# Kernel tuning notes

Hardware: AMD Instinct MI355X
Metric: run time of the kernel (lower is better)

Reference implementation:

```python
import jax, jax.numpy as jnp
import numpy as np

V = 512          # num vertices
F = 64           # pair-feature dim (gpnn_channels in)
C = 64           # gpnn_channels out
E = 8192         # num edges (avg degree 16)


def setup_inputs() -> dict:
    key = jax.random.key(0)
    k1, k2, k3, k4 = jax.random.split(key, 4)
    alpha = jax.random.normal(k1, (V * V, F), dtype=jnp.float32)          # pair features, row v*V+w
    edge_index = jax.random.randint(k2, (2, E), 0, V)                      # COO [src; dst]
    # GPNNEdgeConv.nn = MLP([F, C, C], act='relu')  (norm treated as identity / eval stats)
    w1 = jax.random.normal(k3, (F, C), dtype=jnp.float32) * (1.0 / np.sqrt(F))
    b1 = jnp.zeros((C,), dtype=jnp.float32)
    w2 = jax.random.normal(k4, (C, C), dtype=jnp.float32) * (1.0 / np.sqrt(C))
    b2 = jnp.zeros((C,), dtype=jnp.float32)
    eps = jnp.asarray(0.0, dtype=jnp.float32)                              # train_eps parameter
    return {"alpha": alpha, "edge_index": edge_index,
            "w1": w1, "b1": b1, "w2": w2, "b2": b2, "eps": eps}


def reference(alpha, edge_index, w1, b1, w2, b2, eps):
    # Dense 0/1 adjacency adj_t: adj[v, j] = 1 iff edge j -> v (dst-indexed, as spmm(adj_t, .)).
    adj = jnp.zeros((V, V), dtype=alpha.dtype).at[edge_index[1], edge_index[0]].set(1.0)
    a3 = alpha.reshape(V, V, F)  # a3[v, j] = alpha[v*V + j]
    # message_and_aggregate: out[v*V+w] = row v of spmm(adj_t, A_{v,w}),
    # where A_{v,w}[j] = alpha[v*V+j] + alpha[w*V+j]  (sum aggregation)
    #   = sum_j adj[v,j] * (a3[v,j] + a3[w,j]) = S[v] + T[v,w]
    S = jnp.einsum('vj,vjf->vf', adj, a3)    # [V, F]
    T = jnp.einsum('vj,wjf->vwf', adj, a3)   # [V, V, F]
    out = (S[:, None, :] + T).reshape(V * V, F)
    # GINConv residual: out + (1 + eps) * x_r, then MLP (Linear-ReLU-Linear)
    out = out + (1.0 + eps) * alpha
    h = jax.nn.relu(out @ w1 + b1)
    return h @ w2 + b2
```

## Files before the change

kernel.cpp:

```cpp
#include <hip/hip_runtime.h>
#include <hip/hip_bf16.h>

#define NV 512
#define NF 64

typedef __attribute__((ext_vector_type(8))) short bf16x8;
typedef __attribute__((ext_vector_type(4))) float f32x4;

union BF8 { bf16x8 v; unsigned u[4]; };

__device__ __forceinline__ unsigned short f2bf(float x) {
    unsigned u = __float_as_uint(x);
    unsigned r = (u + 0x7fffu + ((u >> 16) & 1u)) >> 16;
    return (unsigned short)r;
}

__device__ __forceinline__ unsigned awt_addr(int f, int jbyte) {
    return (unsigned)((f * 1024 + jbyte) ^ (((f ^ (f >> 3)) & 7) << 4));
}
__device__ __forceinline__ unsigned wt_addr(int m, int n, int kbyte) {
    return (unsigned)(m * 8192 + ((n * 128 + kbyte) ^ (((n ^ (n >> 3)) & 7) << 4)));
}

__global__ void k_edges(const int* __restrict__ ei, int E, unsigned int* __restrict__ mask) {
    int e = blockIdx.x * 256 + threadIdx.x;
    if (e < E) {
        int s = ei[e];
        int d = ei[E + e];
        atomicOr(&mask[d * 16 + (s >> 5)], 1u << (s & 31));
    }
}

__global__ void k_S(const unsigned int* __restrict__ mask, const float* __restrict__ alpha,
                    float* __restrict__ S) {
    __shared__ float red[4][64];
    int v = blockIdx.x;
    int lane = threadIdx.x & 63;
    int g = threadIdx.x >> 6;
    float a0 = 0.f, a1 = 0.f;
    for (int wd = g * 4; wd < g * 4 + 4; ++wd) {
        unsigned bits = mask[v * 16 + wd];
        while (bits) {
            int b0 = __ffs(bits) - 1; bits &= bits - 1;
            float x0 = alpha[((size_t)v * NV + wd * 32 + b0) * NF + lane];
            if (bits) {
                int b1 = __ffs(bits) - 1; bits &= bits - 1;
                a1 += alpha[((size_t)v * NV + wd * 32 + b1) * NF + lane];
            }
            a0 += x0;
        }
    }
    red[g][lane] = a0 + a1;
    __syncthreads();
    if (g == 0)
        S[v * NF + lane] = red[0][lane] + red[1][lane] + red[2][lane] + red[3][lane];
}

#define SCR_OFF 65536

__global__ __launch_bounds__(512, 4) void k_main(
    const float* __restrict__ alpha, const float* __restrict__ w1, const float* __restrict__ b1,
    const float* __restrict__ w2, const float* __restrict__ b2, const float* __restrict__ eps_p,
    const unsigned int* __restrict__ mask, const float* __restrict__ S,
    float* __restrict__ out)
{
    extern __shared__ char smem[];

    const int w    = blockIdx.x;
    const int t    = threadIdx.x;
    const int lane = t & 63;
    const int wid  = t >> 6;
    const int nlo  = lane & 15;
    const int g    = lane >> 4;
    const int mbase = wid * 64;
    const float* src = alpha + (size_t)w * (NV * NF);

    auto stage_half = [&](int i) {
        int task = i * 512 + t;
        int jb = task >> 4;
        int fq = task & 15;
        unsigned ua[4][4];
#pragma unroll
        for (int h = 0; h < 4; ++h) {
            f32x4 r0 = *(const f32x4*)(src + (size_t)(jb * 8 + 2 * h) * NF + fq * 4);
            f32x4 r1 = *(const f32x4*)(src + (size_t)(jb * 8 + 2 * h + 1) * NF + fq * 4);
#pragma unroll
            for (int c = 0; c < 4; ++c)
                ua[c][h] = (unsigned)f2bf(r0[c]) | ((unsigned)f2bf(r1[c]) << 16);
        }
#pragma unroll
        for (int c = 0; c < 4; ++c) {
            BF8 p;
            p.u[0] = ua[c][0]; p.u[1] = ua[c][1]; p.u[2] = ua[c][2]; p.u[3] = ua[c][3];
            *(bf16x8*)(smem + awt_addr(fq * 4 + c, jb * 16)) = p.v;
        }
    };

    f32x4 acc[4][4];

    stage_half(0);

#pragma unroll
    for (int mi = 0; mi < 4; ++mi)
#pragma unroll
        for (int nt = 0; nt < 4; ++nt)
#pragma unroll
            for (int r = 0; r < 4; ++r)
                acc[mi][nt][r] = S[(size_t)(mbase + mi * 16 + g * 4 + r) * NF + nt * 16 + nlo];

    __syncthreads();

    auto gemm_q = [&](int kq) {
        unsigned qw[4][4];
#pragma unroll
        for (int mi = 0; mi < 4; ++mi) {
            const uint4 q = *(const uint4*)(mask + (size_t)(mbase + mi * 16 + nlo) * 16 + kq * 4);
            qw[mi][0] = q.x; qw[mi][1] = q.y; qw[mi][2] = q.z; qw[mi][3] = q.w;
        }
#pragma unroll
        for (int kr = 0; kr < 4; ++kr) {
            const int kk = kq * 4 + kr;
            BF8 afr[4];
#pragma unroll
            for (int mi = 0; mi < 4; ++mi) {
                unsigned byteb = (qw[mi][kr] >> (g * 8)) & 0xFFu;
#pragma unroll
                for (int h = 0; h < 4; ++h) {
                    unsigned b0 = (byteb >> (2 * h)) & 1u;
                    unsigned b1 = (byteb >> (2 * h + 1)) & 1u;
                    afr[mi].u[h] = (b0 ? 0x3F80u : 0u) | (b1 ? 0x3F800000u : 0u);
                }
            }
#pragma unroll
            for (int nt = 0; nt < 4; ++nt) {
                bf16x8 bfr = *(const bf16x8*)(smem + awt_addr(nt * 16 + nlo, kk * 64 + g * 16));
#pragma unroll
                for (int mi = 0; mi < 4; ++mi)
                    acc[mi][nt] = __builtin_amdgcn_mfma_f32_16x16x32_bf16(afr[mi].v, bfr, acc[mi][nt], 0, 0, 0);
            }
        }
    };

    stage_half(1);
    gemm_q(0);
    gemm_q(1);
    __syncthreads();
    gemm_q(2);
    gemm_q(3);
    __syncthreads();

    if (t < 256) {
        int m  = t >> 7;
        int sub = t & 127;
        int jb = sub >> 4;
        int fq = sub & 15;
        const float* wsrc = m ? w2 : w1;
        unsigned ua[4][4];
#pragma unroll
        for (int h = 0; h < 4; ++h) {
            f32x4 r0 = *(const f32x4*)(wsrc + (size_t)(jb * 8 + 2 * h) * NF + fq * 4);
            f32x4 r1 = *(const f32x4*)(wsrc + (size_t)(jb * 8 + 2 * h + 1) * NF + fq * 4);
#pragma unroll
            for (int c = 0; c < 4; ++c)
                ua[c][h] = (unsigned)f2bf(r0[c]) | ((unsigned)f2bf(r1[c]) << 16);
        }
#pragma unroll
        for (int c = 0; c < 4; ++c) {
            BF8 p;
            p.u[0] = ua[c][0]; p.u[1] = ua[c][1]; p.u[2] = ua[c][2]; p.u[3] = ua[c][3];
            *(bf16x8*)(smem + wt_addr(m, fq * 4 + c, jb * 16)) = p.v;
        }
    }
    float b1v[4], b2v[4];
#pragma unroll
    for (int nt = 0; nt < 4; ++nt) {
        b1v[nt] = b1[nt * 16 + nlo];
        b2v[nt] = b2[nt * 16 + nlo];
    }
    const float ceps = 1.0f + eps_p[0];

    __syncthreads();

    char* myscr = smem + SCR_OFF + wid * 2048;
#pragma unroll
    for (int mi = 0; mi < 4; ++mi) {
        int v0 = mbase + mi * 16;

        float rvv[4][4];
#pragma unroll
        for (int nt = 0; nt < 4; ++nt)
#pragma unroll
            for (int r = 0; r < 4; ++r)
                rvv[nt][r] = alpha[((size_t)(v0 + g * 4 + r) * NV + w) * NF + nt * 16 + nlo];

#pragma unroll
        for (int nt = 0; nt < 4; ++nt) {
            int f = nt * 16 + nlo;
#pragma unroll
            for (int r = 0; r < 4; ++r) {
                float pre = acc[mi][nt][r] + ceps * rvv[nt][r];
                int row = g * 4 + r;
                *(unsigned short*)(myscr + row * 128 + ((2 * f) ^ ((row & 7) << 4))) = f2bf(pre);
            }
        }

        bf16x8 a0 = *(const bf16x8*)(myscr + nlo * 128 + ((g * 16) ^ ((nlo & 7) << 4)));
        bf16x8 a1 = *(const bf16x8*)(myscr + nlo * 128 + ((g * 16 + 64) ^ ((nlo & 7) << 4)));
        f32x4 accm[4];
#pragma unroll
        for (int nt = 0; nt < 4; ++nt) {
            bf16x8 wf0 = *(const bf16x8*)(smem + wt_addr(0, nt * 16 + nlo, g * 16));
            bf16x8 wf1 = *(const bf16x8*)(smem + wt_addr(0, nt * 16 + nlo, 64 + g * 16));
            f32x4 z = {0.f, 0.f, 0.f, 0.f};
            z = __builtin_amdgcn_mfma_f32_16x16x32_bf16(a0, wf0, z, 0, 0, 0);
            z = __builtin_amdgcn_mfma_f32_16x16x32_bf16(a1, wf1, z, 0, 0, 0);
            accm[nt] = z;
        }

#pragma unroll
        for (int nt = 0; nt < 4; ++nt)
#pragma unroll
            for (int r = 0; r < 4; ++r) {
                float hv = accm[nt][r] + b1v[nt];
                hv = hv > 0.f ? hv : 0.f;
                int row = g * 4 + r;
                *(unsigned short*)(myscr + row * 128 + ((2 * (nt * 16 + nlo)) ^ ((row & 7) << 4))) = f2bf(hv);
            }

        bf16x8 h0 = *(const bf16x8*)(myscr + nlo * 128 + ((g * 16) ^ ((nlo & 7) << 4)));
        bf16x8 h1 = *(const bf16x8*)(myscr + nlo * 128 + ((g * 16 + 64) ^ ((nlo & 7) << 4)));
#pragma unroll
        for (int nt = 0; nt < 4; ++nt) {
            bf16x8 wf0 = *(const bf16x8*)(smem + wt_addr(1, nt * 16 + nlo, g * 16));
            bf16x8 wf1 = *(const bf16x8*)(smem + wt_addr(1, nt * 16 + nlo, 64 + g * 16));
            f32x4 z = {0.f, 0.f, 0.f, 0.f};
            z = __builtin_amdgcn_mfma_f32_16x16x32_bf16(h0, wf0, z, 0, 0, 0);
            z = __builtin_amdgcn_mfma_f32_16x16x32_bf16(h1, wf1, z, 0, 0, 0);
#pragma unroll
            for (int r = 0; r < 4; ++r) {
                int vv = v0 + g * 4 + r;
                __builtin_nontemporal_store(z[r] + b2v[nt],
                    out + ((size_t)vv * NV + w) * NF + nt * 16 + nlo);
            }
        }
    }
}

extern "C" void kernel_launch(void* const* d_in, const int* in_sizes, int n_in,
                              void* d_out, int out_size, void* d_ws, size_t ws_size,
                              hipStream_t stream) {
    const float* alpha = (const float*)d_in[0];
    const int*   ei    = (const int*)d_in[1];
    const float* w1    = (const float*)d_in[2];
    const float* b1    = (const float*)d_in[3];
    const float* w2    = (const float*)d_in[4];
    const float* b2    = (const float*)d_in[5];
    const float* eps   = (const float*)d_in[6];
    float* out = (float*)d_out;
    int E = in_sizes[1] / 2;

    unsigned int* mask = (unsigned int*)d_ws;
    float* S = (float*)d_ws + 8192;

    hipMemsetAsync(mask, 0, 8192 * sizeof(unsigned int), stream);
    k_edges<<<(E + 255) / 256, 256, 0, stream>>>(ei, E, mask);
    k_S    <<<NV, 256, 0, stream>>>(mask, alpha, S);

    const int smem_bytes = 81920;
    hipFuncSetAttribute(reinterpret_cast<const void*>(k_main),
                        hipFuncAttributeMaxDynamicSharedMemorySize, smem_bytes);
    k_main <<<NV, 512, smem_bytes, stream>>>(alpha, w1, b1, w2, b2, eps, mask, S, out);
}
```

Before: 73.20 us.

## Prefetch residual rows, reswizzle scratch, shrink LDS, use plain output stores

The epilogue now loads the residual alpha rows for the next 16-row tile before processing the current one, so global loads overlap the MFMA work. The scratch area moves to offset 16384, reusing LDS that appears free after the main loop, which cuts dynamic shared memory from 80KB to 64KB and may allow more resident blocks. The scratch swizzle changes to a new slot function meant to reduce bank conflicts on the 2-byte transposing writes. Nontemporal output stores become ordinary stores. The risks are higher register pressure from the double-buffered residual and possible aliasing if the reused LDS region is still live.

```diff
diff --git a/kernel.cpp b/kernel.cpp
--- a/kernel.cpp
+++ b/kernel.cpp
@@ -20,6 +20,9 @@
 }
 __device__ __forceinline__ unsigned wt_addr(int m, int n, int kbyte) {
     return (unsigned)(m * 8192 + ((n * 128 + kbyte) ^ (((n ^ (n >> 3)) & 7) << 4)));
+}
+__device__ __forceinline__ int scr_slot(int row) {
+    return ((row >> 2) ^ ((row & 3) << 1)) & 7;
 }
 
 __global__ void k_edges(const int* __restrict__ ei, int E, unsigned int* __restrict__ mask) {
@@ -56,7 +59,6 @@
         S[v * NF + lane] = red[0][lane] + red[1][lane] + red[2][lane] + red[3][lane];
 }
 
-#define SCR_OFF 65536
 
 __global__ __launch_bounds__(512, 4) void k_main(
     const float* __restrict__ alpha, const float* __restrict__ w1, const float* __restrict__ b1,
@@ -179,33 +181,47 @@
     }
     const float ceps = 1.0f + eps_p[0];
 
-    __syncthreads();
-
-    char* myscr = smem + SCR_OFF + wid * 2048;
+    float rvv[4][4];
+#pragma unroll
+    for (int nt = 0; nt < 4; ++nt)
+#pragma unroll
+        for (int r = 0; r < 4; ++r)
+            rvv[nt][r] = alpha[((size_t)(mbase + g * 4 + r) * NV + w) * NF + nt * 16 + nlo];
+
+    __syncthreads();
+
+    char* myscr = smem + 16384 + wid * 2048;
 #pragma unroll
     for (int mi = 0; mi < 4; ++mi) {
         int v0 = mbase + mi * 16;
 
-        float rvv[4][4];
+        float rvc[4][4];
 #pragma unroll
         for (int nt = 0; nt < 4; ++nt)
 #pragma unroll
-            for (int r = 0; r < 4; ++r)
-                rvv[nt][r] = alpha[((size_t)(v0 + g * 4 + r) * NV + w) * NF + nt * 16 + nlo];
+            for (int r = 0; r < 4; ++r) rvc[nt][r] = rvv[nt][r];
+
+        if (mi < 3) {
+#pragma unroll
+            for (int nt = 0; nt < 4; ++nt)
+#pragma unroll
+                for (int r = 0; r < 4; ++r)
+                    rvv[nt][r] = alpha[((size_t)(v0 + 16 + g * 4 + r) * NV + w) * NF + nt * 16 + nlo];
+        }
 
 #pragma unroll
         for (int nt = 0; nt < 4; ++nt) {
             int f = nt * 16 + nlo;
 #pragma unroll
             for (int r = 0; r < 4; ++r) {
-                float pre = acc[mi][nt][r] + ceps * rvv[nt][r];
+                float pre = acc[mi][nt][r] + ceps * rvc[nt][r];
                 int row = g * 4 + r;
-                *(unsigned short*)(myscr + row * 128 + ((2 * f) ^ ((row & 7) << 4))) = f2bf(pre);
-            }
-        }
-
-        bf16x8 a0 = *(const bf16x8*)(myscr + nlo * 128 + ((g * 16) ^ ((nlo & 7) << 4)));
-        bf16x8 a1 = *(const bf16x8*)(myscr + nlo * 128 + ((g * 16 + 64) ^ ((nlo & 7) << 4)));
+                *(unsigned short*)(myscr + row * 128 + ((2 * f) ^ (scr_slot(row) << 4))) = f2bf(pre);
+            }
+        }
+
+        bf16x8 a0 = *(const bf16x8*)(myscr + nlo * 128 + ((g * 16) ^ (scr_slot(nlo) << 4)));
+        bf16x8 a1 = *(const bf16x8*)(myscr + nlo * 128 + ((g * 16 + 64) ^ (scr_slot(nlo) << 4)));
         f32x4 accm[4];
 #pragma unroll
         for (int nt = 0; nt < 4; ++nt) {
@@ -224,11 +240,11 @@
                 float hv = accm[nt][r] + b1v[nt];
                 hv = hv > 0.f ? hv : 0.f;
                 int row = g * 4 + r;
-                *(unsigned short*)(myscr + row * 128 + ((2 * (nt * 16 + nlo)) ^ ((row & 7) << 4))) = f2bf(hv);
-            }
-
-        bf16x8 h0 = *(const bf16x8*)(myscr + nlo * 128 + ((g * 16) ^ ((nlo & 7) << 4)));
-        bf16x8 h1 = *(const bf16x8*)(myscr + nlo * 128 + ((g * 16 + 64) ^ ((nlo & 7) << 4)));
+                *(unsigned short*)(myscr + row * 128 + ((2 * (nt * 16 + nlo)) ^ (scr_slot(row) << 4))) = f2bf(hv);
+            }
+
+        bf16x8 h0 = *(const bf16x8*)(myscr + nlo * 128 + ((g * 16) ^ (scr_slot(nlo) << 4)));
+        bf16x8 h1 = *(const bf16x8*)(myscr + nlo * 128 + ((g * 16 + 64) ^ (scr_slot(nlo) << 4)));
 #pragma unroll
         for (int nt = 0; nt < 4; ++nt) {
             bf16x8 wf0 = *(const bf16x8*)(smem + wt_addr(1, nt * 16 + nlo, g * 16));
@@ -239,8 +255,7 @@
 #pragma unroll
             for (int r = 0; r < 4; ++r) {
                 int vv = v0 + g * 4 + r;
-                __builtin_nontemporal_store(z[r] + b2v[nt],
-                    out + ((size_t)vv * NV + w) * NF + nt * 16 + nlo);
+                out[((size_t)vv * NV + w) * NF + nt * 16 + nlo] = z[r] + b2v[nt];
             }
         }
     }
@@ -266,7 +281,7 @@
     k_edges<<<(E + 255) / 256, 256, 0, stream>>>(ei, E, mask);
     k_S    <<<NV, 256, 0, stream>>>(mask, alpha, S);
 
-    const int smem_bytes = 81920;
+    const int smem_bytes = 65536;
     hipFuncSetAttribute(reinterpret_cast<const void*>(k_main),
                         hipFuncAttributeMaxDynamicSharedMemorySize, smem_bytes);
     k_main <<<NV, 512, smem_bytes, stream>>>(alpha, w1, b1, w2, b2, eps, mask, S, out);
```

Measured after the change: 65.50 us. 10.5% less time.
